# Kernel tuning notes

Hardware: AMD Instinct MI355X
Metric: run time of the kernel (lower is better)

The kernel has to match this reference:

```python
import jax, jax.numpy as jnp
import numpy as np

B, S, DIM = 4, 2048, 1024
H, DH = 16, 64
INNER = H * DH  # 1024
SCALE = DH ** -0.5
NEG = -10000.0


def setup_inputs() -> dict:
    key = jax.random.key(0)
    k1, k2, k3, k4 = jax.random.split(key, 4)
    x = jax.random.normal(k1, (B, S, DIM), dtype=jnp.float32)
    w_qkv = jax.random.normal(k2, (DIM, 3 * INNER), dtype=jnp.float32) * (DIM ** -0.5)
    w_out = jax.random.normal(k3, (INNER, DIM), dtype=jnp.float32) * (INNER ** -0.5)
    b_out = jax.random.normal(k4, (DIM,), dtype=jnp.float32) * 0.01
    return {"x": x, "w_qkv": w_qkv, "w_out": w_out, "b_out": b_out}


def reference(x, w_qkv, w_out, b_out):
    b, s, _ = x.shape
    qkv = x @ w_qkv                                  # [b, s, 3*inner]
    q, k, v = jnp.split(qkv, 3, axis=-1)
    def heads(t):
        return t.reshape(b, s, H, DH).transpose(0, 2, 1, 3)  # [b, h, s, dh]
    q, k, v = heads(q), heads(k), heads(v)
    sim = jnp.einsum('bhid,bhjd->bhij', q, k)        # [b, h, s, s]
    i = jnp.arange(s)
    mask = jnp.where(i[None, :] <= i[:, None], 0.0, NEG).astype(sim.dtype)
    # NOTE: original scales (sim + mask), so mask bias is -10000*scale
    attn = jax.nn.softmax((sim + mask) * SCALE, axis=-1)
    out = jnp.einsum('bhij,bhjd->bhid', attn, v)     # [b, h, s, dh]
    out = out.transpose(0, 2, 1, 3).reshape(b, s, INNER)
    return out @ w_out + b_out
```

## Files before the change

### kernel.cpp

```cpp
#include <hip/hip_runtime.h>
#include <stdint.h>

typedef unsigned short u16;
typedef uint32_t u32;
typedef __attribute__((ext_vector_type(4))) float f32x4;
typedef __attribute__((ext_vector_type(16))) float f32x16;
typedef __attribute__((ext_vector_type(8))) short bf16x8;
typedef __attribute__((ext_vector_type(4))) u32 u32x4;

#define MFMA16(a,b,c) __builtin_amdgcn_mfma_f32_16x16x32_bf16((a),(b),(c),0,0,0)
#define MFMA32(a,b,c) __builtin_amdgcn_mfma_f32_32x32x16_bf16((a),(b),(c),0,0,0)
#define QSCALE 0.18033688011112042f
#define MASKB  -1803.3688011112042f
#define MBASE  -16.0f

__device__ __forceinline__ u16 f2bf(float f){
  union { float f; uint32_t u; } v; v.f = f;
  uint32_t r = v.u + 0x7fffu + ((v.u >> 16) & 1u);
  return (u16)(r >> 16);
}

__device__ __forceinline__ u32 cvtpk(float lo, float hi){
  u32 r;
  asm volatile("v_cvt_pk_bf16_f32 %0, %1, %2" : "=v"(r) : "v"(lo), "v"(hi));
  return r;
}

__device__ __forceinline__ void plswap(u32 &a, u32 &b){
  auto r = __builtin_amdgcn_permlane32_swap(a, b, false, false);
  union { decltype(r) v; u32 w[2]; } u; u.v = r;
  a = u.w[0]; b = u.w[1];
}

union U4 { u32x4 u; bf16x8 b; };
__device__ __forceinline__ bf16x8 mkfrag(u32 a, u32 b, u32 c, u32 d){
  U4 x; x.u = (u32x4){a,b,c,d}; return x.b;
}

__device__ __forceinline__ void gload16(const void* g, void* l){
  __builtin_amdgcn_global_load_lds(
      (const __attribute__((address_space(1))) void*)g,
      (__attribute__((address_space(3))) void*)l, 16, 0, 0);
}

__global__ __launch_bounds__(256) void cvt_bf16_k(const float* __restrict__ in, u16* __restrict__ out){
  int i = blockIdx.x*256 + threadIdx.x;
  float4 v = reinterpret_cast<const float4*>(in)[i];
  ushort4 o;
  o.x = f2bf(v.x); o.y = f2bf(v.y); o.z = f2bf(v.z); o.w = f2bf(v.w);
  reinterpret_cast<ushort4*>(out)[i] = o;
}

__global__ __launch_bounds__(256) void transpose_cvt_k(const float* __restrict__ in, u16* __restrict__ out,
                                                       int R, int C){
  __shared__ float tile[64][65];
  int c0 = blockIdx.x*64, r0 = blockIdx.y*64;
  int t = threadIdx.x; int cc = t & 63, rr = t >> 6;
  #pragma unroll
  for (int i=0;i<16;++i){ int r = rr + i*4; tile[r][cc] = in[(size_t)(r0+r)*C + c0+cc]; }
  __syncthreads();
  #pragma unroll
  for (int i=0;i<16;++i){ int r = rr + i*4; out[(size_t)(c0+r)*R + r0+cc] = f2bf(tile[cc][r]); }
}

__device__ __forceinline__ void gemm_core(const u16* __restrict__ A, const u16* __restrict__ Bt,
                                          int bm, int bn, char* lds, f32x4 (&acc)[4][4]){
  const int K = 1024;
  int tid = threadIdx.x, w = tid >> 6, l = tid & 63;
  int lrow = l & 15, lg = l >> 4;
  int wm = w >> 1, wn = w & 1;
  const u16* aSrc = A + (size_t)(bm*128 + w*32 + (l>>3))*K + (((l&7)^(l>>3))<<3);
  const u16* bSrc = Bt + (size_t)(bn*128 + w*32 + (l>>3))*K + (((l&7)^(l>>3))<<3);
  char* aDst = lds + w*4096;
  char* bDst = lds + 16384 + w*4096;
  for (int kk = 0; kk < 16; ++kk){
    __syncthreads();
    #pragma unroll
    for (int i=0;i<4;++i) gload16(aSrc + (size_t)i*8*K + kk*64, aDst + i*1024);
    #pragma unroll
    for (int i=0;i<4;++i) gload16(bSrc + (size_t)i*8*K + kk*64, bDst + i*1024);
    __syncthreads();
    #pragma unroll
    for (int ks=0; ks<2; ++ks){
      bf16x8 af[4], bfv[4];
      #pragma unroll
      for (int m=0;m<4;++m){
        int row = wm*64 + m*16 + lrow;
        af[m] = *reinterpret_cast<const bf16x8*>(lds + row*128 + (((ks*4+lg)^(row&7))<<4));
      }
      #pragma unroll
      for (int n=0;n<4;++n){
        int row = wn*64 + n*16 + lrow;
        bfv[n] = *reinterpret_cast<const bf16x8*>(lds + 16384 + row*128 + (((ks*4+lg)^(row&7))<<4));
      }
      #pragma unroll
      for (int m=0;m<4;++m){
        #pragma unroll
        for (int n=0;n<4;++n)
          acc[m][n] = MFMA16(af[m], bfv[n], acc[m][n]);
      }
    }
  }
}

__global__ __launch_bounds__(256,2) void gemm_qkv_k(const u16* __restrict__ A, const u16* __restrict__ Bt,
                                                    u16* __restrict__ qw, u16* __restrict__ kw,
                                                    u16* __restrict__ vtw){
  __shared__ __align__(16) char lds[32768];
  f32x4 acc[4][4];
  #pragma unroll
  for (int m=0;m<4;++m){
    #pragma unroll
    for (int n=0;n<4;++n) acc[m][n] = (f32x4){0.f,0.f,0.f,0.f};
  }
  int id = blockIdx.x + 24*blockIdx.y;
  int nid = (id & 7)*192 + (id >> 3);
  int bn = nid % 24, bm = nid / 24;
  gemm_core(A, Bt, bm, bn, lds, acc);
  int tid = threadIdx.x, w = tid >> 6, l = tid & 63;
  int lrow = l & 15, lg = l >> 4;
  int wm = w >> 1, wn = w & 1;
  const int which = bn >> 3;
  if (which < 2){
    #pragma unroll
    for (int n=0;n<4;++n){
      int gcol = bn*128 + wn*64 + n*16 + lrow;
      int inner = gcol & 1023;
      int h = inner >> 6, d = inner & 63;
      #pragma unroll
      for (int m=0;m<4;++m){
        #pragma unroll
        for (int r=0;r<4;++r){
          int grow = bm*128 + wm*64 + m*16 + lg*4 + r;
          int b = grow >> 11, sq = grow & 2047;
          float v = acc[m][n][r];
          if (which == 0)
            qw[((size_t)((b*16 + h)*2048 + sq))*64 + d] = f2bf(v * QSCALE);
          else
            kw[((size_t)((b*16 + h)*2048 + sq))*64 + d] = f2bf(v);
        }
      }
    }
  } else {
    __syncthreads();
    #pragma unroll
    for (int n=0;n<4;++n){
      int colL = wn*64 + n*16 + lrow;
      int swz = (colL & 7) << 4;
      #pragma unroll
      for (int m=0;m<4;++m){
        int rowL0 = wm*64 + m*16 + lg*4;
        ushort4 p;
        p.x = f2bf(acc[m][n][0]); p.y = f2bf(acc[m][n][1]);
        p.z = f2bf(acc[m][n][2]); p.w = f2bf(acc[m][n][3]);
        *reinterpret_cast<ushort4*>(lds + colL*256 + ((rowL0*2) ^ swz)) = p;
      }
    }
    __syncthreads();
    const int h0 = bn*2 - 32;
    const int grow0 = bm*128;
    const int b = grow0 >> 11, sq0 = grow0 & 2047;
    const int dp = tid >> 1;
    const int half = (tid & 1) * 128;
    const int h = h0 + (dp >> 6), d = dp & 63;
    const int swz = (dp & 7) << 4;
    u16* dst = vtw + ((size_t)((b*16 + h)*64 + d))*2048 + sq0 + half/2;
    #pragma unroll
    for (int i=0;i<8;++i){
      u32x4 v = *reinterpret_cast<const u32x4*>(lds + dp*256 + ((half + i*16) ^ swz));
      *reinterpret_cast<u32x4*>(dst + i*8) = v;
    }
  }
}

__global__ __launch_bounds__(256) void attn_k(const u16* __restrict__ Qw, const u16* __restrict__ Kw,
                                              const u16* __restrict__ VTw, u16* __restrict__ Ow){
  __shared__ __align__(16) char lds[32768];
  const int bh = blockIdx.x;
  const int y = blockIdx.y, yk = y >> 2, ya = y & 3;
  const int qb = (yk == 0) ? (15 - ya) : (yk == 1) ? (8 + ya) : (yk == 2) ? (4 + ya) : (3 - ya);
  const int tid = threadIdx.x, w = tid >> 6, l = tid & 63;
  const int lo = l & 31, hi = l >> 5;
  const size_t base = (size_t)bh * (2048*64);
  const int qw0 = qb*128 + w*32;
  const int q_l = qw0 + lo;

  bf16x8 qa[4];
  {
    const u16* qsrc = Qw + base + (size_t)q_l*64 + hi*8;
    #pragma unroll
    for (int ks=0; ks<4; ++ks) qa[ks] = *reinterpret_cast<const bf16x8*>(qsrc + ks*16);
  }

  const u32 ONE2 = 0x3F803F80u;
  const bf16x8 onesf = mkfrag(ONE2, ONE2, ONE2, ONE2);

  const int srow = tid >> 3;
  const int scs  = (tid & 7) ^ (srow & 7);
  const u16* kS = Kw  + base + (size_t)srow*64   + scs*8;
  const u16* vS = VTw + base + (size_t)srow*2048 + scs*8;

  f32x16 acc0 = {0,0,0,0,0,0,0,0,0,0,0,0,0,0,0,0};
  f32x16 acc1 = {0,0,0,0,0,0,0,0,0,0,0,0,0,0,0,0};
  f32x16 ls   = {0,0,0,0,0,0,0,0,0,0,0,0,0,0,0,0};
  const f32x16 minit = {MBASE,MBASE,MBASE,MBASE,MBASE,MBASE,MBASE,MBASE,
                        MBASE,MBASE,MBASE,MBASE,MBASE,MBASE,MBASE,MBASE};

  const int nt = qb*2 + 2;

  #define STAGE(buf, t) do { \
    int kv0_ = (t)*64; \
    gload16(kS + (size_t)kv0_*64,        lds + (buf)*16384 +     0 + w*1024); \
    gload16(kS + (size_t)(kv0_+32)*64,   lds + (buf)*16384 +  4096 + w*1024); \
    gload16(vS + kv0_,                   lds + (buf)*16384 +  8192 + w*1024); \
    gload16(vS + kv0_ + (size_t)32*2048, lds + (buf)*16384 + 12288 + w*1024); \
  } while(0)

  STAGE(0, 0);
  __syncthreads();

  int cur = 0;
  for (int t = 0; t < nt; ++t){
    if (t+1 < nt){
      if (cur) STAGE(0, t+1); else STAGE(1, t+1);
    }
    const int kv0 = t*64;
    const char* KB = lds + cur*16384;
    const char* VB = KB + 8192;
    if (kv0 + 63 <= qw0){
      f32x16 s0 = minit;
      f32x16 s1 = minit;
      __builtin_amdgcn_s_setprio(1);
      #pragma unroll
      for (int ks=0; ks<4; ++ks){
        int kr0 = lo, kr1 = 32 + lo;
        bf16x8 kf0 = *reinterpret_cast<const bf16x8*>(KB + kr0*128 + ((ks*32 + hi*16) ^ ((kr0&7)<<4)));
        bf16x8 kf1 = *reinterpret_cast<const bf16x8*>(KB + kr1*128 + ((ks*32 + hi*16) ^ ((kr1&7)<<4)));
        s0 = MFMA32(kf0, qa[ks], s0);
        s1 = MFMA32(kf1, qa[ks], s1);
      }
      __builtin_amdgcn_s_setprio(0);
      #pragma unroll
      for (int r=0; r<16; ++r) s0[r] = exp2f(s0[r]);
      #pragma unroll
      for (int r=0; r<16; ++r) s1[r] = exp2f(s1[r]);
      u32 wd0 = cvtpk(s0[0],s0[1]),   wd1 = cvtpk(s0[2],s0[3]);
      u32 wd2 = cvtpk(s0[4],s0[5]),   wd3 = cvtpk(s0[6],s0[7]);
      u32 wd4 = cvtpk(s0[8],s0[9]),   wd5 = cvtpk(s0[10],s0[11]);
      u32 wd6 = cvtpk(s0[12],s0[13]), wd7 = cvtpk(s0[14],s0[15]);
      u32 we0 = cvtpk(s1[0],s1[1]),   we1 = cvtpk(s1[2],s1[3]);
      u32 we2 = cvtpk(s1[4],s1[5]),   we3 = cvtpk(s1[6],s1[7]);
      u32 we4 = cvtpk(s1[8],s1[9]),   we5 = cvtpk(s1[10],s1[11]);
      u32 we6 = cvtpk(s1[12],s1[13]), we7 = cvtpk(s1[14],s1[15]);
      plswap(wd0, wd2); plswap(wd1, wd3); plswap(wd4, wd6); plswap(wd5, wd7);
      plswap(we0, we2); plswap(we1, we3); plswap(we4, we6); plswap(we5, we7);
      bf16x8 pf0 = mkfrag(wd0, wd1, wd2, wd3);
      bf16x8 pf1 = mkfrag(wd4, wd5, wd6, wd7);
      bf16x8 pf2 = mkfrag(we0, we1, we2, we3);
      bf16x8 pf3 = mkfrag(we4, we5, we6, we7);
      __builtin_amdgcn_s_setprio(1);
      {
        int vrow = lo;
        bf16x8 v0 = *reinterpret_cast<const bf16x8*>(VB + vrow*128 + ((      hi*16) ^ ((vrow&7)<<4)));
        bf16x8 v1 = *reinterpret_cast<const bf16x8*>(VB + vrow*128 + (( 32 + hi*16) ^ ((vrow&7)<<4)));
        bf16x8 v2 = *reinterpret_cast<const bf16x8*>(VB + vrow*128 + (( 64 + hi*16) ^ ((vrow&7)<<4)));
        bf16x8 v3 = *reinterpret_cast<const bf16x8*>(VB + vrow*128 + (( 96 + hi*16) ^ ((vrow&7)<<4)));
        acc0 = MFMA32(v0, pf0, acc0);
        acc0 = MFMA32(v1, pf1, acc0);
        acc0 = MFMA32(v2, pf2, acc0);
        acc0 = MFMA32(v3, pf3, acc0);
      }
      {
        int vrow = 32 + lo;
        bf16x8 v0 = *reinterpret_cast<const bf16x8*>(VB + vrow*128 + ((      hi*16) ^ ((vrow&7)<<4)));
        bf16x8 v1 = *reinterpret_cast<const bf16x8*>(VB + vrow*128 + (( 32 + hi*16) ^ ((vrow&7)<<4)));
        bf16x8 v2 = *reinterpret_cast<const bf16x8*>(VB + vrow*128 + (( 64 + hi*16) ^ ((vrow&7)<<4)));
        bf16x8 v3 = *reinterpret_cast<const bf16x8*>(VB + vrow*128 + (( 96 + hi*16) ^ ((vrow&7)<<4)));
        acc1 = MFMA32(v0, pf0, acc1);
        acc1 = MFMA32(v1, pf1, acc1);
        acc1 = MFMA32(v2, pf2, acc1);
        acc1 = MFMA32(v3, pf3, acc1);
      }
      ls = MFMA32(onesf, pf0, ls);
      ls = MFMA32(onesf, pf1, ls);
      ls = MFMA32(onesf, pf2, ls);
      ls = MFMA32(onesf, pf3, ls);
      __builtin_amdgcn_s_setprio(0);
    } else if (kv0 < qw0 + 32){
      #pragma unroll
      for (int t2=0; t2<2; ++t2){
        const int kvs0 = kv0 + t2*32;
        if (kvs0 < qw0 + 32){
          f32x16 s = minit;
          __builtin_amdgcn_s_setprio(1);
          #pragma unroll
          for (int ks=0; ks<4; ++ks){
            int krow = t2*32 + lo;
            bf16x8 kf = *reinterpret_cast<const bf16x8*>(KB + krow*128 + ((ks*32 + hi*16) ^ ((krow&7)<<4)));
            s = MFMA32(kf, qa[ks], s);
          }
          __builtin_amdgcn_s_setprio(0);
          if (kvs0 + 31 > qw0){
            #pragma unroll
            for (int r=0; r<16; ++r){
              int kvg = kvs0 + (r&3) + 8*(r>>2) + 4*hi;
              if (kvg > q_l) s[r] += MASKB;
            }
          }
          #pragma unroll
          for (int r=0; r<16; ++r) s[r] = exp2f(s[r]);
          u32 wd0 = cvtpk(s[0], s[1]),   wd1 = cvtpk(s[2], s[3]);
          u32 wd2 = cvtpk(s[4], s[5]),   wd3 = cvtpk(s[6], s[7]);
          u32 wd4 = cvtpk(s[8], s[9]),   wd5 = cvtpk(s[10], s[11]);
          u32 wd6 = cvtpk(s[12], s[13]), wd7 = cvtpk(s[14], s[15]);
          plswap(wd0, wd2); plswap(wd1, wd3);
          plswap(wd4, wd6); plswap(wd5, wd7);
          bf16x8 pf0 = mkfrag(wd0, wd1, wd2, wd3);
          bf16x8 pf1 = mkfrag(wd4, wd5, wd6, wd7);
          __builtin_amdgcn_s_setprio(1);
          {
            int vrow = lo;
            bf16x8 v0 = *reinterpret_cast<const bf16x8*>(VB + vrow*128 + ((t2*64 +      hi*16) ^ ((vrow&7)<<4)));
            bf16x8 v1 = *reinterpret_cast<const bf16x8*>(VB + vrow*128 + ((t2*64 + 32 + hi*16) ^ ((vrow&7)<<4)));
            acc0 = MFMA32(v0, pf0, acc0);
            acc0 = MFMA32(v1, pf1, acc0);
          }
          {
            int vrow = 32 + lo;
            bf16x8 v0 = *reinterpret_cast<const bf16x8*>(VB + vrow*128 + ((t2*64 +      hi*16) ^ ((vrow&7)<<4)));
            bf16x8 v1 = *reinterpret_cast<const bf16x8*>(VB + vrow*128 + ((t2*64 + 32 + hi*16) ^ ((vrow&7)<<4)));
            acc1 = MFMA32(v0, pf0, acc1);
            acc1 = MFMA32(v1, pf1, acc1);
          }
          ls = MFMA32(onesf, pf0, ls);
          ls = MFMA32(onesf, pf1, ls);
          __builtin_amdgcn_s_setprio(0);
        }
      }
    }
    __syncthreads();
    cur ^= 1;
  }
  #undef STAGE

  char* T = lds + w*4096;
  float inv = 1.0f / ls[0];
  #pragma unroll
  for (int i=0; i<8; ++i){
    int d = (2*i & 3) + 8*(2*i >> 2) + 4*hi;
    u32 wv0 = cvtpk(acc0[2*i]*inv, acc0[2*i+1]*inv);
    *reinterpret_cast<u32*>(T + lo*128 + ((d*2) ^ ((lo&7)<<4))) = wv0;
    u32 wv1 = cvtpk(acc1[2*i]*inv, acc1[2*i+1]*inv);
    *reinterpret_cast<u32*>(T + lo*128 + (((d+32)*2) ^ ((lo&7)<<4))) = wv1;
  }
  __syncthreads();
  const int b = bh >> 4, h = bh & 15;
  #pragma unroll
  for (int i=0; i<4; ++i){
    int q = i*8 + (l>>3), slot = l&7;
    bf16x8 v = *reinterpret_cast<const bf16x8*>(T + q*128 + ((slot*16) ^ ((q&7)<<4)));
    int sq = qb*128 + w*32 + q;
    *reinterpret_cast<bf16x8*>(Ow + ((size_t)(b*2048 + sq))*1024 + h*64 + slot*8) = v;
  }
}

__global__ __launch_bounds__(256,2) void gemm_out_k(const u16* __restrict__ A, const u16* __restrict__ Bt,
                                                    const float* __restrict__ bias_p, float* __restrict__ out){
  __shared__ __align__(16) char lds[32768];
  f32x4 acc[4][4];
  #pragma unroll
  for (int m=0;m<4;++m){
    #pragma unroll
    for (int n=0;n<4;++n) acc[m][n] = (f32x4){0.f,0.f,0.f,0.f};
  }
  int id = blockIdx.x + 8*blockIdx.y;
  int nid = (id & 7)*64 + (id >> 3);
  int bn = nid % 8, bm = nid / 8;
  gemm_core(A, Bt, bm, bn, lds, acc);
  int tid = threadIdx.x, w = tid >> 6, l = tid & 63;
  int lrow = l & 15, lg = l >> 4;
  int wm = w >> 1, wn = w & 1;
  #pragma unroll
  for (int n=0;n<4;++n){
    int gcol = bn*128 + wn*64 + n*16 + lrow;
    float bias = bias_p[gcol];
    #pragma unroll
    for (int m=0;m<4;++m){
      #pragma unroll
      for (int r=0;r<4;++r){
        int grow = bm*128 + wm*64 + m*16 + lg*4 + r;
        out[(size_t)grow*1024 + gcol] = acc[m][n][r] + bias;
      }
    }
  }
}

extern "C" void kernel_launch(void* const* d_in, const int* in_sizes, int n_in,
                              void* d_out, int out_size, void* d_ws, size_t ws_size,
                              hipStream_t stream){
  (void)in_sizes; (void)n_in; (void)out_size; (void)ws_size;
  const float* x     = (const float*)d_in[0];
  const float* w_qkv = (const float*)d_in[1];
  const float* w_out = (const float*)d_in[2];
  const float* b_out = (const float*)d_in[3];
  float* out = (float*)d_out;
  char* ws = (char*)d_ws;
  u16* xb    = (u16*)(ws + 0);
  u16* wqkvT = (u16*)(ws + 16777216);
  u16* woutT = (u16*)(ws + 23068672);
  u16* qw    = (u16*)(ws + 25165824);
  u16* kw    = (u16*)(ws + 41943040);
  u16* vtw   = (u16*)(ws + 58720256);
  u16* attn  = (u16*)(ws + 75497472);

  cvt_bf16_k<<<8192, 256, 0, stream>>>(x, xb);
  transpose_cvt_k<<<dim3(48,16), 256, 0, stream>>>(w_qkv, wqkvT, 1024, 3072);
  transpose_cvt_k<<<dim3(16,16), 256, 0, stream>>>(w_out, woutT, 1024, 1024);
  gemm_qkv_k<<<dim3(24,64), 256, 0, stream>>>(xb, wqkvT, qw, kw, vtw);
  attn_k<<<dim3(64,16), 256, 0, stream>>>(qw, kw, vtw, attn);
  gemm_out_k<<<dim3(8,64), 256, 0, stream>>>(attn, woutT, b_out, out);
}
```

Before: 175.2 us.

## Replace QKV GEMM with 256x256-tile 8-wave double-buffered kernel

The QKV projection GEMM is rewritten as a 512-thread kernel with 256x256 output tiles and 128KB of dynamic LDS, double-buffered. Global prefetch of the next K-slice is interleaved with MFMA phases using explicit barriers and setprio. Blocks are remapped so consecutive tiles land on the same XCD. The V-transpose epilogue now uses per-wave LDS regions. Separately, gemm_out_k's launch bounds are raised to 4 blocks per CU. The goal is higher data reuse and overlap of loads with compute, at the cost of register pressure and only 384 blocks, which limits occupancy and tail balance.

```diff
diff --git a/kernel.cpp b/kernel.cpp
--- a/kernel.cpp
+++ b/kernel.cpp
@@ -61,6 +61,154 @@
   __syncthreads();
   #pragma unroll
   for (int i=0;i<16;++i){ int r = rr + i*4; out[(size_t)(c0+r)*R + r0+cc] = f2bf(tile[cc][r]); }
+}
+
+__global__ __launch_bounds__(512,1) void gemm_qkv8_k(const u16* __restrict__ A, const u16* __restrict__ Bt,
+                                                     u16* __restrict__ qw, u16* __restrict__ kw,
+                                                     u16* __restrict__ vtw){
+  extern __shared__ char lds[];
+  const int tid = threadIdx.x, w = tid >> 6, l = tid & 63;
+  const int lrow = l & 15, lg = l >> 4;
+  const int wr = w >> 2, wc = w & 3;
+  const int K = 1024;
+  const int id = blockIdx.x;
+  const int xcd = id & 7, s = id >> 3;
+  const int bm = xcd*4 + s/12;
+  const int bn = s % 12;
+
+  const int r0 = tid >> 3;
+  const int c8 = (tid & 7) ^ (r0 & 7);
+  const u16* aS0 = A  + (size_t)(bm*256 +       r0)*K + c8*8;
+  const u16* aS1 = A  + (size_t)(bm*256 +  64 + r0)*K + c8*8;
+  const u16* aS2 = A  + (size_t)(bm*256 + 128 + r0)*K + c8*8;
+  const u16* aS3 = A  + (size_t)(bm*256 + 192 + r0)*K + c8*8;
+  const u16* bS0 = Bt + (size_t)(bn*256 +       r0)*K + c8*8;
+  const u16* bS1 = Bt + (size_t)(bn*256 +  64 + r0)*K + c8*8;
+  const u16* bS2 = Bt + (size_t)(bn*256 + 128 + r0)*K + c8*8;
+  const u16* bS3 = Bt + (size_t)(bn*256 + 192 + r0)*K + c8*8;
+
+  #define STAGE_A4(D, t) do{ \
+    gload16(aS0 + (size_t)(t)*64, (D) +     0 + w*1024); \
+    gload16(aS1 + (size_t)(t)*64, (D) +  8192 + w*1024); \
+    gload16(aS2 + (size_t)(t)*64, (D) + 16384 + w*1024); \
+    gload16(aS3 + (size_t)(t)*64, (D) + 24576 + w*1024); }while(0)
+  #define STAGE_B4(D, t) do{ \
+    gload16(bS0 + (size_t)(t)*64, (D) + 32768 +     0 + w*1024); \
+    gload16(bS1 + (size_t)(t)*64, (D) + 32768 +  8192 + w*1024); \
+    gload16(bS2 + (size_t)(t)*64, (D) + 32768 + 16384 + w*1024); \
+    gload16(bS3 + (size_t)(t)*64, (D) + 32768 + 24576 + w*1024); }while(0)
+
+  f32x4 acc[8][4];
+  #pragma unroll
+  for (int m=0;m<8;++m){
+    #pragma unroll
+    for (int n=0;n<4;++n) acc[m][n] = (f32x4){0.f,0.f,0.f,0.f};
+  }
+  bf16x8 af[4], bf[4];
+
+  #define LDA(mh, ks) do{ \
+    _Pragma("unroll") \
+    for (int m=0;m<4;++m){ \
+      int row = wr*128 + (mh)*64 + m*16 + lrow; \
+      af[m] = *reinterpret_cast<const bf16x8*>(AB + row*128 + ((((ks)*4+lg) ^ (row&7))<<4)); } }while(0)
+  #define LDB(ks) do{ \
+    _Pragma("unroll") \
+    for (int n=0;n<4;++n){ \
+      int row = wc*64 + n*16 + lrow; \
+      bf[n] = *reinterpret_cast<const bf16x8*>(BB + row*128 + ((((ks)*4+lg) ^ (row&7))<<4)); } }while(0)
+  #define MM(mh) do{ \
+    __builtin_amdgcn_s_setprio(1); \
+    _Pragma("unroll") \
+    for (int m=0;m<4;++m){ \
+      _Pragma("unroll") \
+      for (int n=0;n<4;++n) acc[(mh)*4+m][n] = MFMA16(af[m], bf[n], acc[(mh)*4+m][n]); } \
+    __builtin_amdgcn_s_setprio(0); }while(0)
+  #define BAR asm volatile("s_barrier" ::: "memory")
+
+  #define TILE(CURB, DSTB, t, PF) do{ \
+    const char* AB = lds + (CURB); \
+    const char* BB = lds + (CURB) + 32768; \
+    char* D = lds + (DSTB); (void)D; \
+    LDB(0); LDA(0,0); \
+    if (PF) STAGE_A4(D, (t)+1); \
+    BAR; MM(0); BAR; \
+    LDA(1,0); \
+    if (PF) STAGE_B4(D, (t)+1); \
+    BAR; MM(1); BAR; \
+    LDB(1); LDA(0,1); \
+    BAR; MM(0); BAR; \
+    LDA(1,1); \
+    BAR; MM(1); \
+    asm volatile("s_waitcnt vmcnt(0)" ::: "memory"); \
+    BAR; \
+  }while(0)
+
+  STAGE_A4(lds, 0); STAGE_B4(lds, 0);
+  asm volatile("s_waitcnt vmcnt(0)" ::: "memory");
+  __syncthreads();
+
+  #pragma unroll 1
+  for (int tt = 0; tt < 8; ++tt){
+    int t0 = tt*2;
+    TILE(0, 65536, t0, 1);
+    TILE(65536, 0, t0+1, (t0+1) < 15);
+  }
+  #undef TILE
+  #undef MM
+  #undef LDA
+  #undef LDB
+  #undef STAGE_A4
+  #undef STAGE_B4
+
+  const int which = bn >> 2;
+  if (which < 2){
+    #pragma unroll
+    for (int n=0;n<4;++n){
+      int gcol = bn*256 + wc*64 + n*16 + lrow;
+      int inner = gcol & 1023;
+      int h = inner >> 6, d = inner & 63;
+      #pragma unroll
+      for (int m=0;m<8;++m){
+        #pragma unroll
+        for (int r=0;r<4;++r){
+          int grow = bm*256 + wr*128 + m*16 + lg*4 + r;
+          int b = grow >> 11, sq = grow & 2047;
+          float v = acc[m][n][r];
+          if (which == 0)
+            qw[((size_t)((b*16 + h)*2048 + sq))*64 + d] = f2bf(v * QSCALE);
+          else
+            kw[((size_t)((b*16 + h)*2048 + sq))*64 + d] = f2bf(v);
+        }
+      }
+    }
+  } else {
+    char* Wv = lds + w*16384;
+    #pragma unroll
+    for (int n=0;n<4;++n){
+      int dcol = n*16 + lrow;
+      int swz = (dcol & 7) << 4;
+      #pragma unroll
+      for (int m=0;m<8;++m){
+        int rowL = m*16 + lg*4;
+        ushort4 p;
+        p.x = f2bf(acc[m][n][0]); p.y = f2bf(acc[m][n][1]);
+        p.z = f2bf(acc[m][n][2]); p.w = f2bf(acc[m][n][3]);
+        *reinterpret_cast<ushort4*>(Wv + dcol*256 + ((rowL*2) ^ swz)) = p;
+      }
+    }
+    asm volatile("s_waitcnt lgkmcnt(0)" ::: "memory");
+    __builtin_amdgcn_sched_barrier(0);
+    const int grow0 = bm*256 + wr*128;
+    const int b = grow0 >> 11, sq0 = grow0 & 2047;
+    #pragma unroll
+    for (int i=0;i<16;++i){
+      int dcol = i*4 + (l>>4);
+      u32x4 v = *reinterpret_cast<const u32x4*>(Wv + dcol*256 + (((l&15)*16) ^ ((dcol&7)<<4)));
+      int innerd = (bn-8)*256 + wc*64 + dcol;
+      int h = innerd >> 6, d = innerd & 63;
+      *reinterpret_cast<u32x4*>(vtw + ((size_t)((b*16 + h)*64 + d))*2048 + sq0 + (l&15)*8) = v;
+    }
+  }
 }
 
 __device__ __forceinline__ void gemm_core(const u16* __restrict__ A, const u16* __restrict__ Bt,
@@ -99,76 +247,6 @@
         for (int n=0;n<4;++n)
           acc[m][n] = MFMA16(af[m], bfv[n], acc[m][n]);
       }
-    }
-  }
-}
-
-__global__ __launch_bounds__(256,2) void gemm_qkv_k(const u16* __restrict__ A, const u16* __restrict__ Bt,
-                                                    u16* __restrict__ qw, u16* __restrict__ kw,
-                                                    u16* __restrict__ vtw){
-  __shared__ __align__(16) char lds[32768];
-  f32x4 acc[4][4];
-  #pragma unroll
-  for (int m=0;m<4;++m){
-    #pragma unroll
-    for (int n=0;n<4;++n) acc[m][n] = (f32x4){0.f,0.f,0.f,0.f};
-  }
-  int id = blockIdx.x + 24*blockIdx.y;
-  int nid = (id & 7)*192 + (id >> 3);
-  int bn = nid % 24, bm = nid / 24;
-  gemm_core(A, Bt, bm, bn, lds, acc);
-  int tid = threadIdx.x, w = tid >> 6, l = tid & 63;
-  int lrow = l & 15, lg = l >> 4;
-  int wm = w >> 1, wn = w & 1;
-  const int which = bn >> 3;
-  if (which < 2){
-    #pragma unroll
-    for (int n=0;n<4;++n){
-      int gcol = bn*128 + wn*64 + n*16 + lrow;
-      int inner = gcol & 1023;
-      int h = inner >> 6, d = inner & 63;
-      #pragma unroll
-      for (int m=0;m<4;++m){
-        #pragma unroll
-        for (int r=0;r<4;++r){
-          int grow = bm*128 + wm*64 + m*16 + lg*4 + r;
-          int b = grow >> 11, sq = grow & 2047;
-          float v = acc[m][n][r];
-          if (which == 0)
-            qw[((size_t)((b*16 + h)*2048 + sq))*64 + d] = f2bf(v * QSCALE);
-          else
-            kw[((size_t)((b*16 + h)*2048 + sq))*64 + d] = f2bf(v);
-        }
-      }
-    }
-  } else {
-    __syncthreads();
-    #pragma unroll
-    for (int n=0;n<4;++n){
-      int colL = wn*64 + n*16 + lrow;
-      int swz = (colL & 7) << 4;
-      #pragma unroll
-      for (int m=0;m<4;++m){
-        int rowL0 = wm*64 + m*16 + lg*4;
-        ushort4 p;
-        p.x = f2bf(acc[m][n][0]); p.y = f2bf(acc[m][n][1]);
-        p.z = f2bf(acc[m][n][2]); p.w = f2bf(acc[m][n][3]);
-        *reinterpret_cast<ushort4*>(lds + colL*256 + ((rowL0*2) ^ swz)) = p;
-      }
-    }
-    __syncthreads();
-    const int h0 = bn*2 - 32;
-    const int grow0 = bm*128;
-    const int b = grow0 >> 11, sq0 = grow0 & 2047;
-    const int dp = tid >> 1;
-    const int half = (tid & 1) * 128;
-    const int h = h0 + (dp >> 6), d = dp & 63;
-    const int swz = (dp & 7) << 4;
-    u16* dst = vtw + ((size_t)((b*16 + h)*64 + d))*2048 + sq0 + half/2;
-    #pragma unroll
-    for (int i=0;i<8;++i){
-      u32x4 v = *reinterpret_cast<const u32x4*>(lds + dp*256 + ((half + i*16) ^ swz));
-      *reinterpret_cast<u32x4*>(dst + i*8) = v;
     }
   }
 }
@@ -364,7 +442,7 @@
   }
 }
 
-__global__ __launch_bounds__(256,2) void gemm_out_k(const u16* __restrict__ A, const u16* __restrict__ Bt,
+__global__ __launch_bounds__(256,4) void gemm_out_k(const u16* __restrict__ A, const u16* __restrict__ Bt,
                                                     const float* __restrict__ bias_p, float* __restrict__ out){
   __shared__ __align__(16) char lds[32768];
   f32x4 acc[4][4];
@@ -413,10 +491,13 @@
   u16* vtw   = (u16*)(ws + 58720256);
   u16* attn  = (u16*)(ws + 75497472);
 
+  hipFuncSetAttribute((const void*)gemm_qkv8_k,
+                      hipFuncAttributeMaxDynamicSharedMemorySize, 131072);
+
   cvt_bf16_k<<<8192, 256, 0, stream>>>(x, xb);
   transpose_cvt_k<<<dim3(48,16), 256, 0, stream>>>(w_qkv, wqkvT, 1024, 3072);
   transpose_cvt_k<<<dim3(16,16), 256, 0, stream>>>(w_out, woutT, 1024, 1024);
-  gemm_qkv_k<<<dim3(24,64), 256, 0, stream>>>(xb, wqkvT, qw, kw, vtw);
+  gemm_qkv8_k<<<384, 512, 131072, stream>>>(xb, wqkvT, qw, kw, vtw);
   attn_k<<<dim3(64,16), 256, 0, stream>>>(qw, kw, vtw, attn);
   gemm_out_k<<<dim3(8,64), 256, 0, stream>>>(attn, woutT, b_out, out);
 }
```

New measurement: 176.0 us. No clear change (+0.5%).
